# Performance work log

Hardware: AMD Instinct MI355X
Metric: run time of the kernel (lower is better)

## Reference

```python
import jax, jax.numpy as jnp
import numpy as np

N = 65536      # nodes
E = 1048576    # edges (avg degree 16)
L = 24         # input_length == lstm input size == lstm num_layers
H = 64         # lstm hidden


def _lin_init(key, fi, fo):
    return jax.random.normal(key, (fi, fo), jnp.float32) / np.sqrt(fi)


def setup_inputs() -> dict:
    key = jax.random.key(0)
    ks = iter(jax.random.split(key, 64))
    d = {}
    d["x"] = jax.random.normal(next(ks), (N, 421 + L), jnp.float32)
    d["edge_index"] = jax.random.randint(next(ks), (2, E), 0, N)

    def lin(fi, fo):
        return _lin_init(next(ks), fi, fo), jnp.zeros((fo,), jnp.float32)

    d["poi1_W"], d["poi1_b"] = lin(13, 64)
    d["poi2_W"], d["poi2_b"] = lin(64, 64)
    d["svi1_W"], d["svi1_b"] = lin(365, 128)
    d["svi2_W"], d["svi2_b"] = lin(128, 128)
    d["all1_W"], d["all1_b"] = lin(192, 128)
    d["all2_W"], d["all2_b"] = lin(128, 128)
    for name, fi, fo in (("gat1", 128, 128), ("gat2", 128, 128), ("gat3", 128, 64)):
        d[name + "_W"], d[name + "_b"] = lin(fi, fo)
        d[name + "_asrc"] = jax.random.normal(next(ks), (fo,), jnp.float32) / np.sqrt(fo)
        d[name + "_adst"] = jax.random.normal(next(ks), (fo,), jnp.float32) / np.sqrt(fo)
    d["lstm_Wih0"] = jax.random.normal(next(ks), (L, 4 * H), jnp.float32) / np.sqrt(L)
    d["lstm_Wih"] = jax.random.normal(next(ks), (L - 1, H, 4 * H), jnp.float32) / np.sqrt(H)
    d["lstm_Whh"] = jax.random.normal(next(ks), (L, H, 4 * H), jnp.float32) / np.sqrt(H)
    d["lstm_b"] = jnp.zeros((L, 4 * H), jnp.float32)
    d["time1_W"], d["time1_b"] = lin(64, 64)
    d["time2_W"], d["time2_b"] = lin(64, 64)
    d["lin1_W"], d["lin1_b"] = lin(128, 64)
    d["lin2_W"], d["lin2_b"] = lin(64, 64)
    d["lin3_W"], d["lin3_b"] = lin(64, 1)
    return d


def _gat(h_in, W, a_src, a_dst, b, src, dst, n):
    # PyG GATConv (1 head): gather -> per-edge attn -> segment softmax -> scatter
    h = h_in @ W                                   # [N, F]
    s = h @ a_src                                  # [N]
    t = h @ a_dst                                  # [N]
    e = jax.nn.leaky_relu(s[src] + t[dst], 0.2)    # [E']
    m = jax.ops.segment_max(e, dst, num_segments=n)
    ee = jnp.exp(e - m[dst])
    denom = jax.ops.segment_sum(ee, dst, num_segments=n)
    alpha = ee / denom[dst]
    out = jax.ops.segment_sum(h[src] * alpha[:, None], dst, num_segments=n)
    return out + b


def _forward(x, poi1_W, poi1_b, poi2_W, poi2_b, svi1_W, svi1_b, svi2_W, svi2_b,
             all1_W, all1_b, all2_W, all2_b,
             gat1_W, gat1_b, gat1_asrc, gat1_adst,
             gat2_W, gat2_b, gat2_asrc, gat2_adst,
             gat3_W, gat3_b, gat3_asrc, gat3_adst,
             lstm_Wih0, lstm_Wih, lstm_Whh, lstm_b,
             time1_W, time1_b, time2_W, time2_b,
             lin1_W, lin1_b, lin2_W, lin2_b, lin3_W, lin3_b,
             edge_index):
    n = x.shape[0]
    relu = jax.nn.relu
    # feature-branch MLPs
    x_poi = relu(relu(x[:, 3:16] @ poi1_W + poi1_b) @ poi2_W + poi2_b)
    x_svi = relu(relu(x[:, 56:421] @ svi1_W + svi1_b) @ svi2_W + svi2_b)
    h = jnp.concatenate([x_poi, x_svi], axis=1)
    h = relu(relu(h @ all1_W + all1_b) @ all2_W + all2_b)
    # add self loops once (PyG GATConv default add_self_loops=True)
    loops = jnp.arange(n, dtype=edge_index.dtype)
    src = jnp.concatenate([edge_index[0], loops])
    dst = jnp.concatenate([edge_index[1], loops])
    h = relu(_gat(h, gat1_W, gat1_asrc, gat1_adst, gat1_b, src, dst, n))
    h = relu(_gat(h, gat2_W, gat2_asrc, gat2_adst, gat2_b, src, dst, n))
    h = relu(_gat(h, gat3_W, gat3_asrc, gat3_adst, gat3_b, src, dst, n))
    # stacked LSTM over the single timestep t (h0=c0=0 -> f gate & Whh contribute 0)
    inp = x[:, 421:]                               # [N, L]
    hs = []
    for l in range(L):
        Wih = lstm_Wih0 if l == 0 else lstm_Wih[l - 1]
        gates = inp @ Wih + lstm_b[l]              # [N, 4H], torch gate order i,f,g,o
        i, f, g, o = jnp.split(gates, 4, axis=-1)
        c = jax.nn.sigmoid(i) * jnp.tanh(g)
        h_l = jax.nn.sigmoid(o) * jnp.tanh(c)
        hs.append(h_l)
        inp = h_l
    t = hs[2]                                      # hn[2]
    t = relu(relu(t @ time1_W + time1_b) @ time2_W + time2_b)
    z = jnp.concatenate([h, t], axis=1)            # [N, 128]
    z = relu(z @ lin1_W + lin1_b)
    z = relu(z @ lin2_W + lin2_b)
    return z @ lin3_W + lin3_b                     # [N, 1]


def reference(x, edge_index, poi1_W, poi1_b, poi2_W, poi2_b, svi1_W, svi1_b,
              svi2_W, svi2_b, all1_W, all1_b, all2_W, all2_b,
              gat1_W, gat1_b, gat1_asrc, gat1_adst,
              gat2_W, gat2_b, gat2_asrc, gat2_adst,
              gat3_W, gat3_b, gat3_asrc, gat3_adst,
              lstm_Wih0, lstm_Wih, lstm_Whh, lstm_b,
              time1_W, time1_b, time2_W, time2_b,
              lin1_W, lin1_b, lin2_W, lin2_b, lin3_W, lin3_b):
    return _forward(x, poi1_W, poi1_b, poi2_W, poi2_b, svi1_W, svi1_b, svi2_W, svi2_b,
                    all1_W, all1_b, all2_W, all2_b,
                    gat1_W, gat1_b, gat1_asrc, gat1_adst,
                    gat2_W, gat2_b, gat2_asrc, gat2_adst,
                    gat3_W, gat3_b, gat3_asrc, gat3_adst,
                    lstm_Wih0, lstm_Wih, lstm_Whh, lstm_b,
                    time1_W, time1_b, time2_W, time2_b,
                    lin1_W, lin1_b, lin2_W, lin2_b, lin3_W, lin3_b,
                    edge_index)
```

## Files before the change

kernel.cpp:

```cpp
#include <hip/hip_runtime.h>
#include <math.h>

#define DEV __device__ __forceinline__

typedef __attribute__((ext_vector_type(8))) short short8;
typedef __attribute__((ext_vector_type(4))) float f32x4;
typedef float f32x4u __attribute__((ext_vector_type(4), aligned(4)));
typedef __attribute__((ext_vector_type(4))) unsigned int u32x4;
typedef __attribute__((ext_vector_type(4))) _Float16 h16x4;

#define NEG_BIG (-3.0e38f)
#define CAPB 4096
#define CHUNK 4096

DEV float sigm(float x) { return 1.0f / (1.0f + __expf(-x)); }
DEV float leaky(float e) { return (e >= 0.0f) ? e : 0.2f * e; }

DEV void split_bf16(const float f[8], short8& hi, short8& lo) {
#pragma unroll
  for (int i = 0; i < 8; ++i) {
    unsigned u = __builtin_bit_cast(unsigned, f[i]);
    hi[i] = (short)(u >> 16);
    float h = __builtin_bit_cast(float, u & 0xffff0000u);
    float r = f[i] - h;
    lo[i] = (short)(__builtin_bit_cast(unsigned, r) >> 16);
  }
}

DEV unsigned packsplit(float v) {
  unsigned u = __builtin_bit_cast(unsigned, v);
  unsigned hf = u & 0xffff0000u;
  float r = v - __builtin_bit_cast(float, hf);
  return hf | (__builtin_bit_cast(unsigned, r) >> 16);
}

DEV void unpack_pk(const u32x4 p0, const u32x4 p1, short8& hi, short8& lo) {
  u32x4 h, l;
  h[0] = __builtin_amdgcn_perm(p0[1], p0[0], 0x07060302u);
  h[1] = __builtin_amdgcn_perm(p0[3], p0[2], 0x07060302u);
  h[2] = __builtin_amdgcn_perm(p1[1], p1[0], 0x07060302u);
  h[3] = __builtin_amdgcn_perm(p1[3], p1[2], 0x07060302u);
  l[0] = __builtin_amdgcn_perm(p0[1], p0[0], 0x05040100u);
  l[1] = __builtin_amdgcn_perm(p0[3], p0[2], 0x05040100u);
  l[2] = __builtin_amdgcn_perm(p1[1], p1[0], 0x05040100u);
  l[3] = __builtin_amdgcn_perm(p1[3], p1[2], 0x05040100u);
  hi = __builtin_bit_cast(short8, h);
  lo = __builtin_bit_cast(short8, l);
}


__global__ void fill_i32_kernel(int* p, int v, int n) {
  int i = blockIdx.x * blockDim.x + threadIdx.x;
  if (i < n) p[i] = v;
}


__global__ __launch_bounds__(256) void bucket_bin(
    const int* __restrict__ ei, int* __restrict__ bucket_cnt,
    unsigned* __restrict__ ebuf, int E, int Et) {
  __shared__ unsigned stage[CHUNK];
  __shared__ int hist[512], rbase[512], lcur[512];
  const int tid = threadIdx.x;
  const long long e0 = (long long)blockIdx.x * CHUNK;
  const int nalive = (int)((Et - e0) < CHUNK ? (Et - e0) : CHUNK);
  for (int i = tid; i < 512; i += 256) hist[i] = 0;
  __syncthreads();
  for (int k = tid; k < nalive; k += 256) {
    long long e = e0 + k;
    int s, d;
    if (e < E) { s = ei[e]; d = ei[E + e]; } else { s = (int)(e - E); d = s; }
    unsigned p = (unsigned)s | ((unsigned)d << 16);
    stage[k] = p;
    atomicAdd(&hist[d >> 7], 1);
  }
  __syncthreads();
  for (int i = tid; i < 512; i += 256) {
    int c = hist[i];
    rbase[i] = c ? atomicAdd(&bucket_cnt[i], c) : 0;
    lcur[i] = 0;
  }
  __syncthreads();
  for (int k = tid; k < nalive; k += 256) {
    unsigned p = stage[k];
    int b = (int)(p >> 23);
    int lofs = atomicAdd(&lcur[b], 1);
    int pos = rbase[b] + lofs;
    if (pos < CAPB) ebuf[(long long)b * CAPB + pos] = p;
  }
}

__global__ __launch_bounds__(512) void bucket_scan(
    const int* __restrict__ cnt, int* __restrict__ start, int Et) {
  __shared__ int sh[512];
  int tid = threadIdx.x;
  int v = cnt[tid];
  sh[tid] = v;
  __syncthreads();
  int val = v;
  for (int off = 1; off < 512; off <<= 1) {
    int add = (tid >= off) ? sh[tid - off] : 0;
    __syncthreads();
    val += add;
    sh[tid] = val;
    __syncthreads();
  }
  start[tid] = val - v;
  if (tid == 511) start[512] = Et;
}

__global__ __launch_bounds__(128) void bucket_csr(
    const unsigned* __restrict__ ebuf, const int* __restrict__ bucket_cnt,
    const int* __restrict__ bucket_start, int* __restrict__ row_start,
    int* __restrict__ srcs, int N, int Et) {
  __shared__ unsigned stage[CAPB];
  __shared__ int hist[128], hbase[128], lcur[128];
  const int b = blockIdx.x, tid = threadIdx.x;
  int cnt = bucket_cnt[b];
  cnt = cnt < CAPB ? cnt : CAPB;
  const int gbase = bucket_start[b];
  hist[tid] = 0;
  __syncthreads();
  const unsigned* eb = ebuf + (long long)b * CAPB;
  for (int k = tid; k < cnt; k += 128) {
    unsigned p = eb[k];
    stage[k] = p;
    atomicAdd(&hist[(p >> 16) & 127], 1);
  }
  __syncthreads();
  int v = hist[tid];
  hbase[tid] = v;
  __syncthreads();
  int val = v;
  for (int off = 1; off < 128; off <<= 1) {
    int add = (tid >= off) ? hbase[tid - off] : 0;
    __syncthreads();
    val += add;
    hbase[tid] = val;
    __syncthreads();
  }
  int ex = val - v;
  row_start[b * 128 + tid] = gbase + ex;
  __syncthreads();
  hbase[tid] = ex;
  lcur[tid] = 0;
  __syncthreads();
  for (int k = tid; k < cnt; k += 128) {
    unsigned p = stage[k];
    int o = (p >> 16) & 127;
    int lofs = atomicAdd(&lcur[o], 1);
    srcs[gbase + hbase[o] + lofs] = (int)(p & 0xffffu);
  }
  if (b == 0 && tid == 0) row_start[N] = Et;
}

struct WJobs {
  const float* W[16];
  short* hi[16];
  short* lo[16];
  int K[16];
  int M16[16];
  int ldw[16];
  int skip[16];
  int tile0[16];
};

__global__ __launch_bounds__(64) void wsplit_all(WJobs jb, int njobs) {
  int b = blockIdx.x;
  int ji = 0;
#pragma unroll
  for (int i = 1; i < 16; ++i)
    if (i < njobs && b >= jb.tile0[i]) ji = i;
  int t = b - jb.tile0[ji];
  int M16 = jb.M16[ji];
  int kc = t / M16, ntG = t % M16;
  int K = jb.K[ji], ldw = jb.ldw[ji];
  const float* __restrict__ W = jb.W[ji];

  int lane = threadIdx.x;
  int kb = kc * 32 + (lane >> 4) * 8;
  int c = ntG * 16 + (lane & 15);
  if (jb.skip[ji] && c >= 64) c += 64;
  float f[8];
#pragma unroll
  for (int j = 0; j < 8; ++j) {
    int k = kb + j;
    f[j] = (k < K) ? W[(long long)k * ldw + c] : 0.0f;
  }
  short8 h, l;
  split_bf16(f, h, l);
  long long off = ((long long)t * 64 + lane) * 8;
  *(short8*)(jb.hi[ji] + off) = h;
  *(short8*)(jb.lo[ji] + off) = l;
}

template <int MT, int NT, int APK, int OPK, int STE>
__global__ __launch_bounds__(64) void gemm_mfma(
    const void* __restrict__ Av, int lda,
    const short* __restrict__ wh, const short* __restrict__ wl,
    const float* __restrict__ bias,
    void* __restrict__ Cv, int ldc,
    int K, int KC, int act,
    const float* __restrict__ asrc, const float* __restrict__ adst,
    float* __restrict__ sOut, float* __restrict__ tOut) {
  const int lane = threadIdx.x;
  const int m = lane & 15, q = lane >> 4;
  const long long r0 = (long long)blockIdx.x * (MT * 16);

  f32x4 acc[MT][NT];
#pragma unroll
  for (int i = 0; i < MT; ++i)
#pragma unroll
    for (int j = 0; j < NT; ++j) acc[i][j] = (f32x4)(0.0f);

  u32x4 pA[MT][2];
  float fA[MT][8];

  auto loadA = [&](int kc) {
#pragma unroll
    for (int mt = 0; mt < MT; ++mt) {
      if (APK == 1) {
        const unsigned* ap =
            (const unsigned*)Av + (r0 + mt * 16 + m) * lda + kc * 32 + q * 8;
        pA[mt][0] = *(const u32x4*)ap;
        pA[mt][1] = *(const u32x4*)(ap + 4);
      } else {
        const float* ap =
            (const float*)Av + (r0 + mt * 16 + m) * lda + kc * 32 + q * 8;
        if (kc * 32 + 32 <= K) {
          f32x4u p0 = *(const f32x4u*)ap;
          f32x4u p1 = *(const f32x4u*)(ap + 4);
#pragma unroll
          for (int j = 0; j < 4; ++j) { fA[mt][j] = p0[j]; fA[mt][4 + j] = p1[j]; }
        } else {
#pragma unroll
          for (int j = 0; j < 8; ++j) {
            int k = kc * 32 + q * 8 + j;
            fA[mt][j] = (k < K) ? ap[j] : 0.0f;
          }
        }
      }
    }
  };

  loadA(0);
  for (int kc = 0; kc < KC; ++kc) {
    short8 ah[MT], al[MT];
#pragma unroll
    for (int mt = 0; mt < MT; ++mt) {
      if (APK == 1)
        unpack_pk(pA[mt][0], pA[mt][1], ah[mt], al[mt]);
      else
        split_bf16(fA[mt], ah[mt], al[mt]);
    }
    const int kn = (kc + 1 < KC) ? kc + 1 : kc;
#pragma unroll
    for (int g = 0; g < NT / 4; ++g) {
      short8 bh[4], bl[4];
#pragma unroll
      for (int j = 0; j < 4; ++j) {
        long long off = (((long long)kc * NT + (g * 4 + j)) * 64 + lane) * 8;
        bh[j] = *(const short8*)(wh + off);
        bl[j] = *(const short8*)(wl + off);
      }
      if (g == 0) loadA(kn);
#pragma unroll
      for (int mt = 0; mt < MT; ++mt)
#pragma unroll
        for (int j = 0; j < 4; ++j) {
          int nt = g * 4 + j;
          acc[mt][nt] = __builtin_amdgcn_mfma_f32_16x16x32_bf16(ah[mt], bh[j], acc[mt][nt], 0, 0, 0);
          acc[mt][nt] = __builtin_amdgcn_mfma_f32_16x16x32_bf16(ah[mt], bl[j], acc[mt][nt], 0, 0, 0);
          acc[mt][nt] = __builtin_amdgcn_mfma_f32_16x16x32_bf16(al[mt], bh[j], acc[mt][nt], 0, 0, 0);
        }
    }
  }

  if (STE == 2) {
    float w3[NT], bs[NT];
#pragma unroll
    for (int nt = 0; nt < NT; ++nt) {
      int col = nt * 16 + m;
      w3[nt] = asrc[col];
      bs[nt] = bias[col];
    }
#pragma unroll
    for (int mt = 0; mt < MT; ++mt)
#pragma unroll
      for (int reg = 0; reg < 4; ++reg) {
        float ps = 0.0f;
#pragma unroll
        for (int nt = 0; nt < NT; ++nt) {
          float v = fmaxf(acc[mt][nt][reg] + bs[nt], 0.0f);
          ps = fmaf(v, w3[nt], ps);
        }
#pragma unroll
        for (int off = 1; off < 16; off <<= 1) ps += __shfl_xor(ps, off, 64);
        if (m == 0) sOut[r0 + mt * 16 + q * 4 + reg] = ps + adst[0];
      }
    return;
  }

#pragma unroll
  for (int nt = 0; nt < NT; ++nt) {
    int col = nt * 16 + m;
    float bsv = bias ? bias[col] : 0.0f;
#pragma unroll
    for (int mt = 0; mt < MT; ++mt) {
      long long rb = r0 + mt * 16 + q * 4;
#pragma unroll
      for (int reg = 0; reg < 4; ++reg) {
        float v = acc[mt][nt][reg] + bsv;
        if (act == 1) v = fmaxf(v, 0.0f);
        if (OPK == 1)
          ((unsigned*)Cv)[(rb + reg) * ldc + col] = packsplit(v);
        else if (OPK == 2)
          ((_Float16*)Cv)[(rb + reg) * ldc + col] = (_Float16)v;
        else
          ((float*)Cv)[(rb + reg) * ldc + col] = v;
      }
    }
  }

  if (STE == 1) {
    float as[NT], ad[NT];
#pragma unroll
    for (int nt = 0; nt < NT; ++nt) {
      int col = nt * 16 + m;
      as[nt] = asrc[col];
      ad[nt] = adst[col];
    }
#pragma unroll
    for (int mt = 0; mt < MT; ++mt)
#pragma unroll
      for (int reg = 0; reg < 4; ++reg) {
        float ps = 0.0f, pt = 0.0f;
#pragma unroll
        for (int nt = 0; nt < NT; ++nt) {
          ps = fmaf(acc[mt][nt][reg], as[nt], ps);
          pt = fmaf(acc[mt][nt][reg], ad[nt], pt);
        }
#pragma unroll
        for (int off = 1; off < 16; off <<= 1) {
          ps += __shfl_xor(ps, off, 64);
          pt += __shfl_xor(pt, off, 64);
        }
        if (m == 0) {
          long long r = r0 + mt * 16 + q * 4 + reg;
          sOut[r] = ps;
          tOut[r] = pt;
        }
      }
  }
}

template <int APK>
__global__ __launch_bounds__(64) void gemm_lstm(
    const void* __restrict__ Av, int lda,
    const short* __restrict__ wh, const short* __restrict__ wl,
    const float* __restrict__ bias,
    unsigned* __restrict__ H,
    int K, int KC) {
  const int lane = threadIdx.x;
  const int m = lane & 15, q = lane >> 4;
  const long long r0 = (long long)blockIdx.x * 16;

  f32x4 acc[12];
#pragma unroll
  for (int j = 0; j < 12; ++j) acc[j] = (f32x4)(0.0f);

  u32x4 pA[2];
  float fA[8];

  auto loadA = [&](int kc) {
    if (APK == 1) {
      const unsigned* ap = (const unsigned*)Av + (r0 + m) * lda + kc * 32 + q * 8;
      pA[0] = *(const u32x4*)ap;
      pA[1] = *(const u32x4*)(ap + 4);
    } else {
      const float* ap = (const float*)Av + (r0 + m) * lda + kc * 32 + q * 8;
      if (kc * 32 + 32 <= K) {
        f32x4u p0 = *(const f32x4u*)ap;
        f32x4u p1 = *(const f32x4u*)(ap + 4);
#pragma unroll
        for (int j = 0; j < 4; ++j) { fA[j] = p0[j]; fA[4 + j] = p1[j]; }
      } else {
#pragma unroll
        for (int j = 0; j < 8; ++j) {
          int k = kc * 32 + q * 8 + j;
          fA[j] = (k < K) ? ap[j] : 0.0f;
        }
      }
    }
  };

  loadA(0);
  for (int kc = 0; kc < KC; ++kc) {
    short8 ah, al;
    if (APK == 1)
      unpack_pk(pA[0], pA[1], ah, al);
    else
      split_bf16(fA, ah, al);
    const int kn = (kc + 1 < KC) ? kc + 1 : kc;
#pragma unroll
    for (int nt = 0; nt < 12; ++nt) {
      long long off = (((long long)kc * 12 + nt) * 64 + lane) * 8;
      short8 bh = *(const short8*)(wh + off);
      short8 bl = *(const short8*)(wl + off);
      if (nt == 0) loadA(kn);
      acc[nt] = __builtin_amdgcn_mfma_f32_16x16x32_bf16(ah, bh, acc[nt], 0, 0, 0);
      acc[nt] = __builtin_amdgcn_mfma_f32_16x16x32_bf16(ah, bl, acc[nt], 0, 0, 0);
      acc[nt] = __builtin_amdgcn_mfma_f32_16x16x32_bf16(al, bh, acc[nt], 0, 0, 0);
    }
  }

#pragma unroll
  for (int nt = 0; nt < 4; ++nt) {
    int col = nt * 16 + m;
    float bi = bias[col], bg = bias[128 + col], bo = bias[192 + col];
#pragma unroll
    for (int reg = 0; reg < 4; ++reg) {
      float gi = acc[nt][reg] + bi;
      float gg = acc[nt + 4][reg] + bg;
      float go = acc[nt + 8][reg] + bo;
      float cc = sigm(gi) * tanhf(gg);
      H[(r0 + q * 4 + reg) * 64 + col] = packsplit(sigm(go) * tanhf(cc));
    }
  }
}


template <int FO, int OPK>
__global__ __launch_bounds__(256) void gat_agg(
    const _Float16* __restrict__ G, const float* __restrict__ s,
    const float* __restrict__ t, const int* __restrict__ row_start,
    const int* __restrict__ srcs, const float* __restrict__ bias,
    void* __restrict__ outv, int ldc) {
  constexpr int CAP = 128;
  constexpr int LPE = FO / 4;
  constexpr int EPW = 64 / LPE;
  __shared__ float ecache[4][CAP];
  __shared__ int icache[4][CAP];
  const int wv = threadIdx.x >> 6;
  const int lane = threadIdx.x & 63;
  const int d = blockIdx.x * 4 + wv;
  const int start = row_start[d], end = row_start[d + 1];
  const float td = t[d];

  float m = NEG_BIG, dsum = 0.0f;
  for (int j = start + lane; j < end; j += 64) {
    int sj = srcs[j];
    float e = leaky(s[sj] + td);
    int idx = j - start;
    if (idx < CAP) { ecache[wv][idx] = e; icache[wv][idx] = sj; }
    float mn = fmaxf(m, e);
    dsum = dsum * __expf(m - mn) + __expf(e - mn);
    m = mn;
  }
#pragma unroll
  for (int off = 32; off; off >>= 1) {
    float mo = __shfl_xor(m, off, 64);
    float dso = __shfl_xor(dsum, off, 64);
    float mn = fmaxf(m, mo);
    dsum = dsum * __expf(m - mn) + dso * __expf(mo - mn);
    m = mn;
  }
  const float inv = 1.0f / dsum;

  const int deg = end - start;
  const int capdeg = deg < CAP ? deg : CAP;
  for (int idx = lane; idx < capdeg; idx += 64)
    ecache[wv][idx] = __expf(ecache[wv][idx] - m) * inv;
  __syncthreads();

  const int grp = lane / LPE, cl = lane % LPE;
  const _Float16* __restrict__ Gc = G + cl * 4;
  float a0 = 0.0f, a1 = 0.0f, a2 = 0.0f, a3 = 0.0f;
  int idx = grp;
  for (; idx + 3 * EPW < capdeg; idx += 4 * EPW) {
    const int i1 = idx + EPW, i2 = idx + 2 * EPW, i3 = idx + 3 * EPW;
    int s0 = icache[wv][idx], s1 = icache[wv][i1];
    int s2 = icache[wv][i2], s3 = icache[wv][i3];
    float l0 = ecache[wv][idx], l1 = ecache[wv][i1];
    float l2 = ecache[wv][i2], l3 = ecache[wv][i3];
    h16x4 g0 = *(const h16x4*)(Gc + (long long)s0 * FO);
    h16x4 g1 = *(const h16x4*)(Gc + (long long)s1 * FO);
    h16x4 g2 = *(const h16x4*)(Gc + (long long)s2 * FO);
    h16x4 g3 = *(const h16x4*)(Gc + (long long)s3 * FO);
    a0 = fmaf(l0, (float)g0[0], a0); a1 = fmaf(l0, (float)g0[1], a1);
    a2 = fmaf(l0, (float)g0[2], a2); a3 = fmaf(l0, (float)g0[3], a3);
    a0 = fmaf(l1, (float)g1[0], a0); a1 = fmaf(l1, (float)g1[1], a1);
    a2 = fmaf(l1, (float)g1[2], a2); a3 = fmaf(l1, (float)g1[3], a3);
    a0 = fmaf(l2, (float)g2[0], a0); a1 = fmaf(l2, (float)g2[1], a1);
    a2 = fmaf(l2, (float)g2[2], a2); a3 = fmaf(l2, (float)g2[3], a3);
    a0 = fmaf(l3, (float)g3[0], a0); a1 = fmaf(l3, (float)g3[1], a1);
    a2 = fmaf(l3, (float)g3[2], a2); a3 = fmaf(l3, (float)g3[3], a3);
  }
  for (; idx + EPW < capdeg; idx += 2 * EPW) {
    const int i1 = idx + EPW;
    int s0 = icache[wv][idx], s1 = icache[wv][i1];
    float l0 = ecache[wv][idx], l1 = ecache[wv][i1];
    h16x4 g0 = *(const h16x4*)(Gc + (long long)s0 * FO);
    h16x4 g1 = *(const h16x4*)(Gc + (long long)s1 * FO);
    a0 = fmaf(l0, (float)g0[0], a0); a1 = fmaf(l0, (float)g0[1], a1);
    a2 = fmaf(l0, (float)g0[2], a2); a3 = fmaf(l0, (float)g0[3], a3);
    a0 = fmaf(l1, (float)g1[0], a0); a1 = fmaf(l1, (float)g1[1], a1);
    a2 = fmaf(l1, (float)g1[2], a2); a3 = fmaf(l1, (float)g1[3], a3);
  }
  for (; idx < capdeg; idx += EPW) {
    int s0 = icache[wv][idx];
    float l0 = ecache[wv][idx];
    h16x4 g0 = *(const h16x4*)(Gc + (long long)s0 * FO);
    a0 = fmaf(l0, (float)g0[0], a0); a1 = fmaf(l0, (float)g0[1], a1);
    a2 = fmaf(l0, (float)g0[2], a2); a3 = fmaf(l0, (float)g0[3], a3);
  }
  for (; idx < deg; idx += EPW) {
    int s0 = srcs[start + idx];
    float l0 = __expf(leaky(s[s0] + td) - m) * inv;
    h16x4 g0 = *(const h16x4*)(Gc + (long long)s0 * FO);
    a0 = fmaf(l0, (float)g0[0], a0); a1 = fmaf(l0, (float)g0[1], a1);
    a2 = fmaf(l0, (float)g0[2], a2); a3 = fmaf(l0, (float)g0[3], a3);
  }
#pragma unroll
  for (int off = 32; off >= LPE; off >>= 1) {
    a0 += __shfl_xor(a0, off, 64);
    a1 += __shfl_xor(a1, off, 64);
    a2 += __shfl_xor(a2, off, 64);
    a3 += __shfl_xor(a3, off, 64);
  }
  if (grp == 0) {
    f32x4u bs = *(const f32x4u*)(bias + cl * 4);
    float v0 = fmaxf(a0 + bs[0], 0.0f);
    float v1 = fmaxf(a1 + bs[1], 0.0f);
    float v2 = fmaxf(a2 + bs[2], 0.0f);
    float v3 = fmaxf(a3 + bs[3], 0.0f);
    if (OPK == 1) {
      u32x4 pv;
      pv[0] = packsplit(v0); pv[1] = packsplit(v1);
      pv[2] = packsplit(v2); pv[3] = packsplit(v3);
      *(u32x4*)((unsigned*)outv + (long long)d * ldc + cl * 4) = pv;
    } else {
      f32x4u v; v[0] = v0; v[1] = v1; v[2] = v2; v[3] = v3;
      *(f32x4u*)((float*)outv + (long long)d * ldc + cl * 4) = v;
    }
  }
}


struct WSplit { const short* hi; const short* lo; };

extern "C" void kernel_launch(void* const* d_in, const int* in_sizes, int n_in,
                              void* d_out, int out_size, void* d_ws, size_t ws_size,
                              hipStream_t stream) {
  const int N = 65536, E = 1048576;
  const int Et = E + N;

  const float* x        = (const float*)d_in[0];
  const int*   ei       = (const int*)d_in[1];
  const float* poi1_W   = (const float*)d_in[2];
  const float* poi1_b   = (const float*)d_in[3];
  const float* poi2_W   = (const float*)d_in[4];
  const float* poi2_b   = (const float*)d_in[5];
  const float* svi1_W   = (const float*)d_in[6];
  const float* svi1_b   = (const float*)d_in[7];
  const float* svi2_W   = (const float*)d_in[8];
  const float* svi2_b   = (const float*)d_in[9];
  const float* all1_W   = (const float*)d_in[10];
  const float* all1_b   = (const float*)d_in[11];
  const float* all2_W   = (const float*)d_in[12];
  const float* all2_b   = (const float*)d_in[13];
  const float* gat1_W   = (const float*)d_in[14];
  const float* gat1_b   = (const float*)d_in[15];
  const float* gat1_as  = (const float*)d_in[16];
  const float* gat1_ad  = (const float*)d_in[17];
  const float* gat2_W   = (const float*)d_in[18];
  const float* gat2_b   = (const float*)d_in[19];
  const float* gat2_as  = (const float*)d_in[20];
  const float* gat2_ad  = (const float*)d_in[21];
  const float* gat3_W   = (const float*)d_in[22];
  const float* gat3_b   = (const float*)d_in[23];
  const float* gat3_as  = (const float*)d_in[24];
  const float* gat3_ad  = (const float*)d_in[25];
  const float* lstm_Wih0= (const float*)d_in[26];
  const float* lstm_Wih = (const float*)d_in[27];
  const float* lstm_b   = (const float*)d_in[29];
  const float* time1_W  = (const float*)d_in[30];
  const float* time1_b  = (const float*)d_in[31];
  const float* time2_W  = (const float*)d_in[32];
  const float* time2_b  = (const float*)d_in[33];
  const float* lin1_W   = (const float*)d_in[34];
  const float* lin1_b   = (const float*)d_in[35];
  const float* lin2_W   = (const float*)d_in[36];
  const float* lin2_b   = (const float*)d_in[37];
  const float* lin3_W   = (const float*)d_in[38];
  const float* lin3_b   = (const float*)d_in[39];
  float* out = (float*)d_out;

  float* wsf   = (float*)d_ws;
  float* R192  = wsf;
  float* RA    = R192 + (size_t)N * 192;
  float* RA2   = RA + (size_t)N * 64;
  float* RB    = RA + (size_t)N * 128;
  float* Rz    = RB + (size_t)N * 256;
  float* sArr  = Rz + (size_t)N * 128;
  float* tArr  = sArr + N;
  int* ints         = (int*)(tArr + N);
  int* row_start    = ints;
  int* srcs         = row_start + (N + 1);
  int* bucket_cnt   = srcs + Et;
  int* bucket_start = bucket_cnt + 512;
  unsigned* ebuf    = (unsigned*)(bucket_start + 513);
  short* pool = (short*)(((uintptr_t)(ebuf + 512 * CAPB) + 15) & ~(uintptr_t)15);

  WJobs jb{};
  int nj = 0, tiles = 0;
  auto split = [&](const float* W, int K, int M, int ldw, int skip) -> WSplit {
    int KC = (K + 31) / 32;
    size_t sz = (size_t)KC * M * 32;
    short* hi = pool; pool += sz;
    short* lo = pool; pool += sz;
    jb.W[nj] = W; jb.hi[nj] = hi; jb.lo[nj] = lo;
    jb.K[nj] = K; jb.M16[nj] = M / 16; jb.ldw[nj] = ldw; jb.skip[nj] = skip;
    jb.tile0[nj] = tiles;
    tiles += KC * (M / 16);
    ++nj;
    return {hi, lo};
  };

  auto gemm = [&](const void* A, int lda, WSplit w, const float* bias,
                  void* C, int ldc, int K, int M, int act, int apk, int opk) {
    int KC = (K + 31) / 32;
    dim3 grid(N / 32), blk(64);
    if (M == 64) {
      if (apk == 0 && opk == 1)
        hipLaunchKernelGGL((gemm_mfma<2, 4, 0, 1, 0>), grid, blk, 0, stream,
                           A, lda, w.hi, w.lo, bias, C, ldc, K, KC, act,
                           nullptr, nullptr, nullptr, nullptr);
      else if (apk == 1 && opk == 1)
        hipLaunchKernelGGL((gemm_mfma<2, 4, 1, 1, 0>), grid, blk, 0, stream,
                           A, lda, w.hi, w.lo, bias, C, ldc, K, KC, act,
                           nullptr, nullptr, nullptr, nullptr);
      else if (apk == 1 && opk == 0)
        hipLaunchKernelGGL((gemm_mfma<2, 4, 1, 0, 0>), grid, blk, 0, stream,
                           A, lda, w.hi, w.lo, bias, C, ldc, K, KC, act,
                           nullptr, nullptr, nullptr, nullptr);
      else
        hipLaunchKernelGGL((gemm_mfma<2, 4, 0, 0, 0>), grid, blk, 0, stream,
                           A, lda, w.hi, w.lo, bias, C, ldc, K, KC, act,
                           nullptr, nullptr, nullptr, nullptr);
    } else {
      if (apk == 0 && opk == 1)
        hipLaunchKernelGGL((gemm_mfma<2, 8, 0, 1, 0>), grid, blk, 0, stream,
                           A, lda, w.hi, w.lo, bias, C, ldc, K, KC, act,
                           nullptr, nullptr, nullptr, nullptr);
      else if (apk == 1 && opk == 1)
        hipLaunchKernelGGL((gemm_mfma<2, 8, 1, 1, 0>), grid, blk, 0, stream,
                           A, lda, w.hi, w.lo, bias, C, ldc, K, KC, act,
                           nullptr, nullptr, nullptr, nullptr);
      else if (apk == 1 && opk == 0)
        hipLaunchKernelGGL((gemm_mfma<2, 8, 1, 0, 0>), grid, blk, 0, stream,
                           A, lda, w.hi, w.lo, bias, C, ldc, K, KC, act,
                           nullptr, nullptr, nullptr, nullptr);
      else
        hipLaunchKernelGGL((gemm_mfma<2, 8, 0, 0, 0>), grid, blk, 0, stream,
                           A, lda, w.hi, w.lo, bias, C, ldc, K, KC, act,
                           nullptr, nullptr, nullptr, nullptr);
    }
  };
  auto gemm_st = [&](const void* A, WSplit w, void* G, int M,
                     const float* as_, const float* ad_) {
    dim3 grid(N / 32), blk(64);
    if (M == 128)
      hipLaunchKernelGGL((gemm_mfma<2, 8, 1, 2, 1>), grid, blk, 0, stream,
                         A, 128, w.hi, w.lo, (const float*)nullptr,
                         G, 128, 128, 4, 0, as_, ad_, sArr, tArr);
    else
      hipLaunchKernelGGL((gemm_mfma<2, 4, 1, 2, 1>), grid, blk, 0, stream,
                         A, 128, w.hi, w.lo, (const float*)nullptr,
                         G, 64, 128, 4, 0, as_, ad_, sArr, tArr);
  };

  WSplit wpoi1 = split(poi1_W, 13, 64, 64, 0);
  WSplit wpoi2 = split(poi2_W, 64, 64, 64, 0);
  WSplit wsvi1 = split(svi1_W, 365, 128, 128, 0);
  WSplit wsvi2 = split(svi2_W, 128, 128, 128, 0);
  WSplit wall1 = split(all1_W, 192, 128, 128, 0);
  WSplit wall2 = split(all2_W, 128, 128, 128, 0);
  WSplit wg1   = split(gat1_W, 128, 128, 128, 0);
  WSplit wg2   = split(gat2_W, 128, 128, 128, 0);
  WSplit wg3   = split(gat3_W, 128, 64, 64, 0);
  WSplit wls0  = split(lstm_Wih0, 24, 192, 256, 1);
  WSplit wls1  = split(lstm_Wih, 64, 192, 256, 1);
  WSplit wls2  = split(lstm_Wih + 64 * 256, 64, 192, 256, 1);
  WSplit wt1   = split(time1_W, 64, 64, 64, 0);
  WSplit wt2   = split(time2_W, 64, 64, 64, 0);
  WSplit wl1   = split(lin1_W, 128, 64, 64, 0);
  WSplit wl2   = split(lin2_W, 64, 64, 64, 0);
  hipLaunchKernelGGL(wsplit_all, dim3(tiles), dim3(64), 0, stream, jb, nj);

  const int TB = 256;

  hipLaunchKernelGGL(fill_i32_kernel, dim3(2), dim3(TB), 0, stream,
                     bucket_cnt, 0, 512);
  hipLaunchKernelGGL(bucket_bin, dim3((Et + CHUNK - 1) / CHUNK), dim3(256),
                     0, stream, ei, bucket_cnt, ebuf, E, Et);
  hipLaunchKernelGGL(bucket_scan, dim3(1), dim3(512), 0, stream,
                     bucket_cnt, bucket_start, Et);
  hipLaunchKernelGGL(bucket_csr, dim3(512), dim3(128), 0, stream,
                     ebuf, bucket_cnt, bucket_start, row_start, srcs, N, Et);

  gemm(x + 3, 445, wpoi1, poi1_b, RA, 64, 13, 64, 1, 0, 1);
  gemm(RA, 64, wpoi2, poi2_b, R192, 192, 64, 64, 1, 1, 1);
  gemm(x + 56, 445, wsvi1, svi1_b, RB, 128, 365, 128, 1, 0, 1);
  gemm(RB, 128, wsvi2, svi2_b, R192 + 64, 192, 128, 128, 1, 1, 1);
  gemm(R192, 192, wall1, all1_b, RA, 128, 192, 128, 1, 1, 1);
  gemm(RA, 128, wall2, all2_b, RB, 128, 128, 128, 1, 1, 1);

  const int aggBlocks = N / 4;
  _Float16* Gh = (_Float16*)RA;

  gemm_st(RB, wg1, Gh, 128, gat1_as, gat1_ad);
  hipLaunchKernelGGL((gat_agg<128, 1>), dim3(aggBlocks), dim3(256), 0, stream,
                     Gh, sArr, tArr, row_start, srcs, gat1_b, RB, 128);
  gemm_st(RB, wg2, Gh, 128, gat2_as, gat2_ad);
  hipLaunchKernelGGL((gat_agg<128, 1>), dim3(aggBlocks), dim3(256), 0, stream,
                     Gh, sArr, tArr, row_start, srcs, gat2_b, RB, 128);
  gemm_st(RB, wg3, Gh, 64, gat3_as, gat3_ad);
  hipLaunchKernelGGL((gat_agg<64, 1>), dim3(aggBlocks), dim3(256), 0, stream,
                     Gh, sArr, tArr, row_start, srcs, gat3_b, Rz, 128);

  hipLaunchKernelGGL((gemm_lstm<0>), dim3(N / 16), dim3(64), 0, stream,
                     x + 421, 445, wls0.hi, wls0.lo, lstm_b,
                     (unsigned*)RA, 24, 1);
  hipLaunchKernelGGL((gemm_lstm<1>), dim3(N / 16), dim3(64), 0, stream,
                     RA, 64, wls1.hi, wls1.lo, lstm_b + 256,
                     (unsigned*)RA2, 64, 2);
  hipLaunchKernelGGL((gemm_lstm<1>), dim3(N / 16), dim3(64), 0, stream,
                     RA2, 64, wls2.hi, wls2.lo, lstm_b + 512,
                     (unsigned*)RA, 64, 2);

  gemm(RA, 64, wt1, time1_b, RA2, 64, 64, 64, 1, 1, 1);
  gemm(RA2, 64, wt2, time2_b, Rz + 64, 128, 64, 64, 1, 1, 1);

  gemm(Rz, 128, wl1, lin1_b, RA, 64, 128, 64, 1, 1, 1);
  hipLaunchKernelGGL((gemm_mfma<2, 4, 1, 0, 2>), dim3(N / 32), dim3(64), 0, stream,
                     RA, 64, wl2.hi, wl2.lo, lin2_b, nullptr, 64, 64, 2, 0,
                     lin3_W, lin3_b, out, nullptr);
}
```

Before: 672.6 us.

## Double-buffer B-fragment register loads in MFMA GEMM and LSTM kernels

```diff
diff --git a/kernel.cpp b/kernel.cpp
--- a/kernel.cpp
+++ b/kernel.cpp
@@ -48,6 +48,23 @@
   lo = __builtin_bit_cast(short8, l);
 }
 
+template <int G, int MT, int NT>
+DEV void mfma_grp(f32x4 (&acc)[MT][NT], const short8 (&ah)[MT],
+                  const short8 (&al)[MT], const short8 (&bh)[4],
+                  const short8 (&bl)[4]) {
+#pragma unroll
+  for (int mt = 0; mt < MT; ++mt)
+#pragma unroll
+    for (int j = 0; j < 4; ++j) {
+      acc[mt][G * 4 + j] = __builtin_amdgcn_mfma_f32_16x16x32_bf16(
+          ah[mt], bh[j], acc[mt][G * 4 + j], 0, 0, 0);
+      acc[mt][G * 4 + j] = __builtin_amdgcn_mfma_f32_16x16x32_bf16(
+          ah[mt], bl[j], acc[mt][G * 4 + j], 0, 0, 0);
+      acc[mt][G * 4 + j] = __builtin_amdgcn_mfma_f32_16x16x32_bf16(
+          al[mt], bh[j], acc[mt][G * 4 + j], 0, 0, 0);
+    }
+}
+
 
 __global__ void fill_i32_kernel(int* p, int v, int n) {
   int i = blockIdx.x * blockDim.x + threadIdx.x;
@@ -242,9 +259,8 @@
     }
   };
 
-  loadA(0);
-  for (int kc = 0; kc < KC; ++kc) {
-    short8 ah[MT], al[MT];
+  short8 ah[MT], al[MT];
+  auto unpackA = [&]() {
 #pragma unroll
     for (int mt = 0; mt < MT; ++mt) {
       if (APK == 1)
@@ -252,26 +268,48 @@
       else
         split_bf16(fA[mt], ah[mt], al[mt]);
     }
-    const int kn = (kc + 1 < KC) ? kc + 1 : kc;
-#pragma unroll
-    for (int g = 0; g < NT / 4; ++g) {
-      short8 bh[4], bl[4];
-#pragma unroll
-      for (int j = 0; j < 4; ++j) {
-        long long off = (((long long)kc * NT + (g * 4 + j)) * 64 + lane) * 8;
-        bh[j] = *(const short8*)(wh + off);
-        bl[j] = *(const short8*)(wl + off);
+  };
+
+  short8 bh0[4], bl0[4], bh1[4], bl1[4];
+  auto loadB = [&](short8 (&bh)[4], short8 (&bl)[4], int kc, int g) {
+#pragma unroll
+    for (int j = 0; j < 4; ++j) {
+      long long off = (((long long)kc * NT + (g * 4 + j)) * 64 + lane) * 8;
+      bh[j] = *(const short8*)(wh + off);
+      bl[j] = *(const short8*)(wl + off);
+    }
+  };
+
+  if constexpr (NT == 4) {
+    loadA(0);
+    loadB(bh0, bl0, 0, 0);
+    int kc = 0;
+    for (; kc + 2 <= KC; kc += 2) {
+      unpackA();
+      loadB(bh1, bl1, kc + 1, 0);
+      loadA(kc + 1);
+      mfma_grp<0, MT, NT>(acc, ah, al, bh0, bl0);
+      unpackA();
+      if (kc + 2 < KC) {
+        loadB(bh0, bl0, kc + 2, 0);
+        loadA(kc + 2);
       }
-      if (g == 0) loadA(kn);
-#pragma unroll
-      for (int mt = 0; mt < MT; ++mt)
-#pragma unroll
-        for (int j = 0; j < 4; ++j) {
-          int nt = g * 4 + j;
-          acc[mt][nt] = __builtin_amdgcn_mfma_f32_16x16x32_bf16(ah[mt], bh[j], acc[mt][nt], 0, 0, 0);
-          acc[mt][nt] = __builtin_amdgcn_mfma_f32_16x16x32_bf16(ah[mt], bl[j], acc[mt][nt], 0, 0, 0);
-          acc[mt][nt] = __builtin_amdgcn_mfma_f32_16x16x32_bf16(al[mt], bh[j], acc[mt][nt], 0, 0, 0);
-        }
+      mfma_grp<0, MT, NT>(acc, ah, al, bh1, bl1);
+    }
+    if (kc < KC) {
+      unpackA();
+      mfma_grp<0, MT, NT>(acc, ah, al, bh0, bl0);
+    }
+  } else {
+    loadA(0);
+    loadB(bh0, bl0, 0, 0);
+    for (int kc = 0; kc < KC; ++kc) {
+      unpackA();
+      loadB(bh1, bl1, kc, 1);
+      if (kc + 1 < KC) loadA(kc + 1);
+      mfma_grp<0, MT, NT>(acc, ah, al, bh0, bl0);
+      if (kc + 1 < KC) loadB(bh0, bl0, kc + 1, 0);
+      mfma_grp<1, MT, NT>(acc, ah, al, bh1, bl1);
     }
   }
 
@@ -393,23 +431,35 @@
     }
   };
 
+  short8 bh0, bl0, bh1, bl1;
+  auto loadB = [&](short8& bh, short8& bl, int kc, int nt) {
+    long long off = (((long long)kc * 12 + nt) * 64 + lane) * 8;
+    bh = *(const short8*)(wh + off);
+    bl = *(const short8*)(wl + off);
+  };
+
   loadA(0);
+  loadB(bh0, bl0, 0, 0);
   for (int kc = 0; kc < KC; ++kc) {
     short8 ah, al;
     if (APK == 1)
       unpack_pk(pA[0], pA[1], ah, al);
     else
       split_bf16(fA, ah, al);
+    loadB(bh1, bl1, kc, 1);
+    if (kc + 1 < KC) loadA(kc + 1);
     const int kn = (kc + 1 < KC) ? kc + 1 : kc;
 #pragma unroll
     for (int nt = 0; nt < 12; ++nt) {
-      long long off = (((long long)kc * 12 + nt) * 64 + lane) * 8;
-      short8 bh = *(const short8*)(wh + off);
-      short8 bl = *(const short8*)(wl + off);
-      if (nt == 0) loadA(kn);
-      acc[nt] = __builtin_amdgcn_mfma_f32_16x16x32_bf16(ah, bh, acc[nt], 0, 0, 0);
-      acc[nt] = __builtin_amdgcn_mfma_f32_16x16x32_bf16(ah, bl, acc[nt], 0, 0, 0);
-      acc[nt] = __builtin_amdgcn_mfma_f32_16x16x32_bf16(al, bh, acc[nt], 0, 0, 0);
+      short8& cbh = (nt & 1) ? bh1 : bh0;
+      short8& cbl = (nt & 1) ? bl1 : bl0;
+      acc[nt] = __builtin_amdgcn_mfma_f32_16x16x32_bf16(ah, cbh, acc[nt], 0, 0, 0);
+      acc[nt] = __builtin_amdgcn_mfma_f32_16x16x32_bf16(ah, cbl, acc[nt], 0, 0, 0);
+      acc[nt] = __builtin_amdgcn_mfma_f32_16x16x32_bf16(al, cbh, acc[nt], 0, 0, 0);
+      if (nt + 2 < 12)
+        loadB((nt & 1) ? bh1 : bh0, (nt & 1) ? bl1 : bl0, kc, nt + 2);
+      else if (nt + 2 == 12)
+        loadB(bh0, bl0, kn, 0);
     }
   }
 
```

Measured after the change: 649.5 us. -3.4%, faster.
